# Kernel optimization log

Measured on AMD Instinct MI355X. Metric: run time of the kernel, lower is better.

## Reference

```python
import jax, jax.numpy as jnp
import numpy as np

TILE = 128
NEG = -1e10


def rotate_half(x):
    half = x.shape[-1] // 2
    return jnp.concatenate([-x[..., half:], x[..., :half]], axis=-1)


def setup_inputs() -> dict:
    key = jax.random.key(0)
    ks = jax.random.split(key, 7)
    B, S, E, H, D, K = 1, 4096, 2048, 16, 128, 8
    T = S // TILE
    x = jax.random.normal(ks[0], (B, S, E), jnp.float32)
    wq = jax.random.normal(ks[1], (E, H * D), jnp.float32) * 0.02
    wk = jax.random.normal(ks[2], (E, H * D), jnp.float32) * 0.02
    wv = jax.random.normal(ks[3], (E, H * D), jnp.float32) * 0.02
    wo = jax.random.normal(ks[4], (H * D, E), jnp.float32) * 0.02
    rope_angles = jax.random.uniform(ks[5], (S, D // 2), jnp.float32)
    anchor_indices = jax.random.randint(ks[6], (B, H, T, K), 0, T).astype(jnp.int32)
    return {"x": x, "wq": wq, "wk": wk, "wv": wv, "wo": wo,
            "rope_angles": rope_angles, "anchor_indices": anchor_indices}


def reference(x, wq, wk, wv, wo, rope_angles, anchor_indices):
    B, S, E = x.shape
    D = rope_angles.shape[1] * 2          # head_dim
    H = wq.shape[1] // D                  # num_heads
    T = S // TILE                         # num_tiles
    sm_scale = 1.0 / jnp.sqrt(jnp.float32(D))

    # QKV projections -> [B, H, S, D]
    def proj(w):
        return (x @ w).reshape(B, S, H, D).transpose(0, 2, 1, 3).astype(jnp.float32)
    q, k, v = proj(wq), proj(wk), proj(wv)

    # RoPE (half-split / rotate_half format)
    cos = jnp.cos(rope_angles)[None, None]   # [1,1,S,D/2]
    sin = jnp.sin(rope_angles)[None, None]
    cos_f = jnp.concatenate([cos, cos], axis=-1)
    sin_f = jnp.concatenate([sin, sin], axis=-1)
    q = q * cos_f + rotate_half(q) * sin_f
    k = k * cos_f + rotate_half(k) * sin_f

    # Tile selection: anchor tiles + local (diagonal) tile -> [B,H,T,K+1]
    local = jnp.broadcast_to(jnp.arange(T, dtype=jnp.int32)[None, None, :, None], (B, H, T, 1))
    tile_sel = jnp.concatenate([anchor_indices, local], axis=-1)
    L = tile_sel.shape[-1] * TILE            # sparse_len
    token_idx = tile_sel[..., None] * TILE + jnp.arange(TILE, dtype=jnp.int32)[None, None, None, None, :]
    flat_idx = jnp.clip(token_idx.reshape(B, H, T, L), 0, S - 1)  # [B,H,T,L]

    # Gather selected KV tiles: [B,H,T,L,D]
    def gather(kv):
        return jnp.take_along_axis(kv, flat_idx.reshape(B, H, T * L, 1), axis=2).reshape(B, H, T, L, D)
    k_sp, v_sp = gather(k), gather(v)

    # Block-sparse attention per query tile
    q_t = q.reshape(B, H, T, TILE, D)
    logits = jnp.einsum('bhtqd,bhtkd->bhtqk', q_t, k_sp) * sm_scale
    q_pos = jnp.arange(S).reshape(T, TILE)
    future = flat_idx[:, :, :, None, :] > q_pos[None, None, :, :, None]  # causal mask on gathered keys
    logits = jnp.where(future, NEG, logits)
    w = jax.nn.softmax(logits, axis=-1)
    all_masked = jnp.all(future, axis=-1, keepdims=True)
    w = jnp.where(all_masked, 0.0, w)
    w = jnp.where(jnp.isnan(w), 0.0, w)
    out = jnp.einsum('bhtqk,bhtkd->bhtqd', w, v_sp)

    out = out.reshape(B, H, S, D).transpose(0, 2, 1, 3).reshape(B, S, H * D)
    return out @ wo
```

## Files before the change

### kernel.cpp

```cpp
#include <hip/hip_runtime.h>
#include <stdint.h>

typedef unsigned short u16;
typedef unsigned int u32;

#define S_LEN 4096
#define EMB 2048
#define NH 16
#define HD 128
#define HDTOT 2048
#define T_TILES 32
#define KANCH 8
#define SM_SCALE 0.088388347648318447f

typedef __bf16 bf16x8 __attribute__((ext_vector_type(8)));
typedef float f32x4 __attribute__((ext_vector_type(4)));

typedef const __attribute__((address_space(1))) u32 ga_u32;
typedef __attribute__((address_space(3))) u32 lds_u32;

__device__ __forceinline__ u16 f2bf(float f) {
  u32 b = __builtin_bit_cast(u32, f);
  b = (b + 0x7FFFu + ((b >> 16) & 1u)) >> 16;
  return (u16)b;
}
__device__ __forceinline__ float bf2f(u16 u) {
  return __builtin_bit_cast(float, ((u32)u) << 16);
}
__device__ __forceinline__ f32x4 mfma16(bf16x8 a, bf16x8 b, f32x4 c) {
  return __builtin_amdgcn_mfma_f32_16x16x32_bf16(a, b, c, 0, 0, 0);
}

#define ASM_LGKM0 do { asm volatile("s_waitcnt lgkmcnt(0)" ::: "memory"); \
                       __builtin_amdgcn_sched_barrier(0); } while (0)
#define ASM_VMC(n) do { asm volatile("s_waitcnt vmcnt(" #n ")" ::: "memory"); \
                        __builtin_amdgcn_sched_barrier(0); } while (0)

__global__ __launch_bounds__(256) void k_convert_x(const float* __restrict__ x,
                                                   u16* __restrict__ xb) {
  int i = (blockIdx.x * 256 + threadIdx.x) * 4;
  float4 v = *(const float4*)(x + i);
  ushort4 o;
  o.x = f2bf(v.x); o.y = f2bf(v.y); o.z = f2bf(v.z); o.w = f2bf(v.w);
  *(ushort4*)(xb + i) = o;
}

__global__ __launch_bounds__(256) void k_transpose_w(
    const float* __restrict__ w0, const float* __restrict__ w1,
    const float* __restrict__ w2, const float* __restrict__ w3,
    u16* __restrict__ o0, u16* __restrict__ o1,
    u16* __restrict__ o2, u16* __restrict__ o3) {
  const float* w; u16* o;
  if (blockIdx.z == 0)      { w = w0; o = o0; }
  else if (blockIdx.z == 1) { w = w1; o = o1; }
  else if (blockIdx.z == 2) { w = w2; o = o2; }
  else                      { w = w3; o = o3; }
  __shared__ float tile[64][68];
  int n0 = blockIdx.x * 64, k0 = blockIdx.y * 64;
  int tid = threadIdx.x;
  int r = tid >> 4, cq = (tid & 15) << 2;
  for (int p = 0; p < 4; ++p) {
    float4 v = *(const float4*)(w + (size_t)(k0 + r + p * 16) * EMB + n0 + cq);
    tile[r + p * 16][cq + 0] = v.x;
    tile[r + p * 16][cq + 1] = v.y;
    tile[r + p * 16][cq + 2] = v.z;
    tile[r + p * 16][cq + 3] = v.w;
  }
  __syncthreads();
  for (int p = 0; p < 4; ++p) {
    int rn = r + p * 16;
    ushort4 u;
    u.x = f2bf(tile[cq + 0][rn]);
    u.y = f2bf(tile[cq + 1][rn]);
    u.z = f2bf(tile[cq + 2][rn]);
    u.w = f2bf(tile[cq + 3][rn]);
    *(ushort4*)(o + (size_t)(n0 + rn) * EMB + k0 + cq) = u;
  }
}

__global__ __launch_bounds__(256) void k_transpose_v(const u16* __restrict__ v,
                                                     u16* __restrict__ vt) {
  __shared__ u16 tile[64][72];
  int n0 = blockIdx.x * 64, s0 = blockIdx.y * 64;
  int tid = threadIdx.x;
  int r = tid >> 4, cq = (tid & 15) << 2;
  for (int p = 0; p < 4; ++p) {
    ushort4 u = *(const ushort4*)(v + (size_t)(s0 + r + p * 16) * HDTOT + n0 + cq);
    tile[r + p * 16][cq + 0] = u.x;
    tile[r + p * 16][cq + 1] = u.y;
    tile[r + p * 16][cq + 2] = u.z;
    tile[r + p * 16][cq + 3] = u.w;
  }
  __syncthreads();
  for (int p = 0; p < 4; ++p) {
    int rn = r + p * 16;
    ushort4 o;
    o.x = tile[cq + 0][rn];
    o.y = tile[cq + 1][rn];
    o.z = tile[cq + 2][rn];
    o.w = tile[cq + 3][rn];
    *(ushort4*)(vt + (size_t)(n0 + rn) * S_LEN + s0 + cq) = o;
  }
}

template <bool BF16OUT>
__device__ __forceinline__ void gemm_body(const u16* __restrict__ A,
                                          const u16* __restrict__ Bt,
                                          void* __restrict__ Cv,
                                          int N, int K, int m0, int n0,
                                          u16* As, u16* Bs) {
  const int tid = threadIdx.x;
  const int lane = tid & 63, wave = tid >> 6;
  const int quad = lane >> 4, l16 = lane & 15;
  const int wm = (wave >> 1) * 64, wn = (wave & 1) * 64;
  f32x4 acc[4][4] = {};

  const int flat0 = wave * 1024 + lane * 16;
  for (int kt = 0; kt < K; kt += 32) {
    for (int half = 0; half < 2; ++half) {
      int flat = flat0 + half * 4096;
      int row = flat >> 6, colb = flat & 63;
      const char* ga = (const char*)A + ((size_t)(m0 + row) * K + kt) * 2 + colb;
      const char* gb = (const char*)Bt + ((size_t)(n0 + row) * K + kt) * 2 + colb;
      int loff = wave * 1024 + half * 4096;
      __builtin_amdgcn_global_load_lds((ga_u32*)ga, (lds_u32*)((char*)As + loff), 16, 0, 0);
      __builtin_amdgcn_global_load_lds((ga_u32*)gb, (lds_u32*)((char*)Bs + loff), 16, 0, 0);
    }
    __syncthreads();
    bf16x8 af[4], bfr[4];
    for (int mt = 0; mt < 4; ++mt)
      af[mt] = *(const bf16x8*)(As + (wm + mt * 16 + l16) * 32 + quad * 8);
    for (int nt = 0; nt < 4; ++nt)
      bfr[nt] = *(const bf16x8*)(Bs + (wn + nt * 16 + l16) * 32 + quad * 8);
    for (int mt = 0; mt < 4; ++mt)
      for (int nt = 0; nt < 4; ++nt)
        acc[mt][nt] = mfma16(af[mt], bfr[nt], acc[mt][nt]);
    __syncthreads();
  }
  for (int mt = 0; mt < 4; ++mt) {
    int row = m0 + wm + mt * 16 + quad * 4;
    for (int nt = 0; nt < 4; ++nt) {
      int col = n0 + wn + nt * 16 + l16;
      for (int r = 0; r < 4; ++r) {
        if (BF16OUT)
          ((u16*)Cv)[(size_t)(row + r) * N + col] = f2bf(acc[mt][nt][r]);
        else
          ((float*)Cv)[(size_t)(row + r) * N + col] = acc[mt][nt][r];
      }
    }
  }
}

template <bool BF16OUT>
__global__ __launch_bounds__(256) void k_gemm(const u16* __restrict__ A,
                                              const u16* __restrict__ Bt,
                                              void* __restrict__ Cv,
                                              int N, int K) {
  __shared__ __align__(16) u16 As[128 * 32];
  __shared__ __align__(16) u16 Bs[128 * 32];
  gemm_body<BF16OUT>(A, Bt, Cv, N, K, blockIdx.y * 128, blockIdx.x * 128, As, Bs);
}

__global__ __launch_bounds__(512, 2) void k_gemm256_qkv(
    const u16* __restrict__ A, const u16* __restrict__ Bt,
    u16* __restrict__ q, u16* __restrict__ k, u16* __restrict__ v) {
  __shared__ __align__(16) u16 lds[65536];
  int flat = blockIdx.y * 24 + blockIdx.x;
  flat = (flat & 7) * 48 + (flat >> 3);
  const int bx = flat % 24, by = flat / 24;
  const int m0 = by * 256;
  const int n0g = bx * 256;
  u16* out = (bx < 8) ? q : ((bx < 16) ? k : v);
  const int ncol0 = (bx & 7) * 256;

  const int tid = threadIdx.x;
  const int lane = tid & 63, wave = tid >> 6;
  const int quad = lane >> 4, l16 = lane & 15;
  const int wm = wave >> 2, wn = wave & 3;
  const int sw0 = (quad ^ (l16 & 7)) * 8, sw1 = ((quad ^ (l16 & 7)) ^ 4) * 8;

  size_t soff[2];
#pragma unroll
  for (int p = 0; p < 2; ++p) {
    int fl = p * 8192 + tid * 16;
    int row = fl >> 7;
    int gsw = ((fl >> 4) & 7) ^ (row & 7);
    soff[p] = (size_t)row * 4096 + (size_t)(gsw * 16);
  }
  const char* aBase = (const char*)A + (size_t)m0 * 4096;
  const char* bBase = (const char*)Bt + (size_t)n0g * 4096;
  const int dstW = wave * 1024;

  auto stA = [&](int buf, int half, int kt) {
#pragma unroll
    for (int p = 0; p < 2; ++p)
      __builtin_amdgcn_global_load_lds(
          (ga_u32*)(aBase + (size_t)half * 524288 + (size_t)kt * 128 + soff[p]),
          (lds_u32*)((char*)lds + buf * 32768 + half * 16384 + p * 8192 + dstW),
          16, 0, 0);
  };
  auto stB = [&](int buf, int half, int kt) {
#pragma unroll
    for (int p = 0; p < 2; ++p)
      __builtin_amdgcn_global_load_lds(
          (ga_u32*)(bBase + (size_t)half * 524288 + (size_t)kt * 128 + soff[p]),
          (lds_u32*)((char*)lds + 65536 + buf * 32768 + half * 16384 + p * 8192 + dstW),
          16, 0, 0);
  };
  const u16* aRd = lds + wm * 8192 + l16 * 64;
  const u16* bRd = lds + 32768 + (wn >> 1) * 8192 + ((wn & 1) * 64 + l16) * 64;

  f32x4 acc[8][4] = {};

  stB(0, 0, 0); stA(0, 0, 0); stB(0, 1, 0); stA(0, 1, 0);
  stB(1, 0, 1); stA(1, 0, 1);
  ASM_VMC(4);
  __builtin_amdgcn_s_barrier();

  const int NT = EMB / 64;
  for (int j = 0; j < NT; ++j) {
    const int par = j & 1;
    const u16* aT = aRd + par * 16384;
    const u16* bT = bRd + par * 16384;
    bf16x8 af[4][2], blo[2][2], bhi[2][2];
#pragma unroll
    for (int m = 0; m < 4; ++m) {
      af[m][0] = *(const bf16x8*)(aT + m * 1024 + sw0);
      af[m][1] = *(const bf16x8*)(aT + m * 1024 + sw1);
    }
#pragma unroll
    for (int n = 0; n < 2; ++n) {
      blo[n][0] = *(const bf16x8*)(bT + n * 1024 + sw0);
      blo[n][1] = *(const bf16x8*)(bT + n * 1024 + sw1);
    }
    if (j + 1 < NT) stB(1 - par, 1, j + 1);
    __builtin_amdgcn_s_barrier();
    ASM_LGKM0;
    __builtin_amdgcn_s_setprio(1);
#pragma unroll
    for (int m = 0; m < 4; ++m)
#pragma unroll
      for (int n = 0; n < 2; ++n) {
        acc[m][n] = mfma16(af[m][0], blo[n][0], acc[m][n]);
        acc[m][n] = mfma16(af[m][1], blo[n][1], acc[m][n]);
      }
    __builtin_amdgcn_s_setprio(0);
    __builtin_amdgcn_s_barrier();
#pragma unroll
    for (int n = 0; n < 2; ++n) {
      bhi[n][0] = *(const bf16x8*)(bT + (n + 2) * 1024 + sw0);
      bhi[n][1] = *(const bf16x8*)(bT + (n + 2) * 1024 + sw1);
    }
    if (j + 1 < NT) stA(1 - par, 1, j + 1);
    __builtin_amdgcn_s_barrier();
    ASM_LGKM0;
    __builtin_amdgcn_s_setprio(1);
#pragma unroll
    for (int m = 0; m < 4; ++m)
#pragma unroll
      for (int n = 0; n < 2; ++n) {
        acc[m][n + 2] = mfma16(af[m][0], bhi[n][0], acc[m][n + 2]);
        acc[m][n + 2] = mfma16(af[m][1], bhi[n][1], acc[m][n + 2]);
      }
    __builtin_amdgcn_s_setprio(0);
    __builtin_amdgcn_s_barrier();
#pragma unroll
    for (int m = 0; m < 4; ++m) {
      af[m][0] = *(const bf16x8*)(aT + (m + 4) * 1024 + sw0);
      af[m][1] = *(const bf16x8*)(aT + (m + 4) * 1024 + sw1);
    }
    if (j + 2 < NT) stB(par, 0, j + 2);
    __builtin_amdgcn_s_barrier();
    ASM_LGKM0;
    __builtin_amdgcn_s_setprio(1);
#pragma unroll
    for (int m = 0; m < 4; ++m)
#pragma unroll
      for (int n = 0; n < 2; ++n) {
        acc[m + 4][n + 2] = mfma16(af[m][0], bhi[n][0], acc[m + 4][n + 2]);
        acc[m + 4][n + 2] = mfma16(af[m][1], bhi[n][1], acc[m + 4][n + 2]);
      }
    __builtin_amdgcn_s_setprio(0);
    __builtin_amdgcn_s_barrier();
    if (j + 2 < NT) stA(par, 0, j + 2);
    __builtin_amdgcn_s_barrier();
    __builtin_amdgcn_s_setprio(1);
#pragma unroll
    for (int m = 0; m < 4; ++m)
#pragma unroll
      for (int n = 0; n < 2; ++n) {
        acc[m + 4][n] = mfma16(af[m][0], blo[n][0], acc[m + 4][n]);
        acc[m + 4][n] = mfma16(af[m][1], blo[n][1], acc[m + 4][n]);
      }
    __builtin_amdgcn_s_setprio(0);
    if (j == NT - 2) { ASM_VMC(0); } else { ASM_VMC(4); }
    __builtin_amdgcn_s_barrier();
  }
#pragma unroll
  for (int m = 0; m < 8; ++m) {
    int row = m0 + wm * 128 + m * 16 + quad * 4;
#pragma unroll
    for (int n = 0; n < 4; ++n) {
      int col = ncol0 + wn * 64 + n * 16 + l16;
#pragma unroll
      for (int r = 0; r < 4; ++r)
        out[(size_t)(row + r) * HDTOT + col] = f2bf(acc[m][n][r]);
    }
  }
}

__global__ __launch_bounds__(256) void k_rope(u16* __restrict__ q, u16* __restrict__ k,
                                              const float* __restrict__ ang) {
  int gid = blockIdx.x * 256 + threadIdx.x;
  int s = gid >> 7;
  int h = (gid >> 3) & (NH - 1);
  int dq = (gid & 7) << 3;
  const float* ap = ang + s * 64 + dq;
  float4 a0 = *(const float4*)(ap);
  float4 a1 = *(const float4*)(ap + 4);
  float sn[8], cs[8];
  __sincosf(a0.x, &sn[0], &cs[0]);
  __sincosf(a0.y, &sn[1], &cs[1]);
  __sincosf(a0.z, &sn[2], &cs[2]);
  __sincosf(a0.w, &sn[3], &cs[3]);
  __sincosf(a1.x, &sn[4], &cs[4]);
  __sincosf(a1.y, &sn[5], &cs[5]);
  __sincosf(a1.z, &sn[6], &cs[6]);
  __sincosf(a1.w, &sn[7], &cs[7]);
  size_t base = (size_t)s * HDTOT + h * HD + dq;
  u16* ptrs[2] = {q, k};
#pragma unroll
  for (int a = 0; a < 2; ++a) {
    u16* p = ptrs[a] + base;
    ushort4 x1a = *(const ushort4*)(p);
    ushort4 x1b = *(const ushort4*)(p + 4);
    ushort4 x2a = *(const ushort4*)(p + 64);
    ushort4 x2b = *(const ushort4*)(p + 68);
    u16 v1[8] = {x1a.x, x1a.y, x1a.z, x1a.w, x1b.x, x1b.y, x1b.z, x1b.w};
    u16 v2[8] = {x2a.x, x2a.y, x2a.z, x2a.w, x2b.x, x2b.y, x2b.z, x2b.w};
    u16 o1[8], o2[8];
#pragma unroll
    for (int e = 0; e < 8; ++e) {
      float f1 = bf2f(v1[e]), f2 = bf2f(v2[e]);
      o1[e] = f2bf(f1 * cs[e] - f2 * sn[e]);
      o2[e] = f2bf(f2 * cs[e] + f1 * sn[e]);
    }
    *(ushort4*)(p)      = make_ushort4(o1[0], o1[1], o1[2], o1[3]);
    *(ushort4*)(p + 4)  = make_ushort4(o1[4], o1[5], o1[6], o1[7]);
    *(ushort4*)(p + 64) = make_ushort4(o2[0], o2[1], o2[2], o2[3]);
    *(ushort4*)(p + 68) = make_ushort4(o2[4], o2[5], o2[6], o2[7]);
  }
}

__device__ __forceinline__ bf16x8 ldsfrag(const u16* __restrict__ sbuf, int r, int cb) {
  return *(const bf16x8*)(sbuf + r * 128 + (((cb ^ (r & 15)) << 3)));
}
__device__ __forceinline__ bf16x8 ldsfragV(const u16* __restrict__ sbuf, int r, int cb) {
  return *(const bf16x8*)(sbuf + r * 64 + (((cb ^ (r & 7)) << 3)));
}

__global__ __launch_bounds__(512, 4) void k_attn(const u16* __restrict__ q,
                                                 const u16* __restrict__ k,
                                                 const u16* __restrict__ vt,
                                                 const int* __restrict__ anch,
                                                 u16* __restrict__ out) {
  __shared__ __align__(16) u16 bufK[2][64 * 128];
  __shared__ __align__(16) u16 bufV[2][128 * 64];
  __shared__ int s_tj[KANCH + 1];
  __shared__ int s_nv;
  const int xx = blockIdx.x, yy = blockIdx.y;
  const int h = (yy & 7) | ((xx & 1) << 3);
  const int t = (yy & 8) ? ((xx >> 1) << 1) : (T_TILES - 1 - ((xx >> 1) << 1));
  const int tid = threadIdx.x;
  const int lane = tid & 63, wave = tid >> 6;
  const int quad = lane >> 4, l16 = lane & 15;
  const int wq0 = wave * 16;

  int offK[2], offV[2];
#pragma unroll
  for (int p = 0; p < 2; ++p) {
    int krow = (wave * 2 + p) * 4 + (lane >> 4);
    int kcol = ((lane & 15) ^ (krow & 15)) << 3;
    offK[p] = (krow * HDTOT + kcol) * 2;
    int vrow = (wave * 2 + p) * 8 + (lane >> 3);
    int vcol = ((lane & 7) ^ (vrow & 7)) << 3;
    offV[p] = (vrow * S_LEN + vcol) * 2;
  }

  if (tid == 0) {
    int nv = 0;
    for (int j = 0; j < KANCH; ++j) {
      int tj = anch[((h * T_TILES) + t) * KANCH + j];
      if (tj <= t) s_tj[nv++] = tj;
    }
    s_tj[nv++] = t;
    s_nv = nv;
  }

  {
    const char* gq = (const char*)(q + (size_t)(t * 128) * HDTOT + h * HD);
    char* lq = (char*)bufK + wave * 4096;
#pragma unroll
    for (int p = 0; p < 4; ++p) {
      int qrow = (wave * 4 + p) * 4 + (lane >> 4);
      int qcol = ((lane & 15) ^ (qrow & 15)) << 3;
      __builtin_amdgcn_global_load_lds((ga_u32*)(gq + (qrow * HDTOT + qcol) * 2),
                                       (lds_u32*)(lq + p * 1024), 16, 0, 0);
    }
  }
  __syncthreads();

  bf16x8 qf[4];
#pragma unroll
  for (int ks = 0; ks < 4; ++ks)
    qf[ks] = ldsfrag(&bufK[0][0], wq0 + l16, ks * 4 + quad);

  const int nv2 = 2 * s_nv;
  const char* kh = (const char*)(k + h * HD);
  const char* vh = (const char*)(vt + (size_t)(h * HD) * S_LEN);

  __syncthreads();

  {
    int key0 = s_tj[0] * 128;
    const char* gk = kh + (size_t)key0 * (HDTOT * 2);
    const char* gv = vh + (size_t)key0 * 2;
    char* lk = (char*)bufK[0] + wave * 2048;
    char* lv = (char*)bufV[0] + wave * 2048;
#pragma unroll
    for (int p = 0; p < 2; ++p) {
      __builtin_amdgcn_global_load_lds((ga_u32*)(gk + offK[p]),
                                       (lds_u32*)(lk + p * 1024), 16, 0, 0);
      __builtin_amdgcn_global_load_lds((ga_u32*)(gv + offV[p]),
                                       (lds_u32*)(lv + p * 1024), 16, 0, 0);
    }
  }

  f32x4 oacc[8] = {};
  float m_st = -1e30f, l_st = 0.f;

  for (int i = 0; i < nv2; ++i) {
    const int par = i & 1;
    const u16* K_c = bufK[par];
    const u16* V_c = bufV[par];
    const int tj = s_tj[i >> 1];
    const int half = i & 1;
    const bool diag = (tj == t);

    __syncthreads();

    if (i + 1 < nv2) {
      int inx = i + 1;
      int key0 = s_tj[inx >> 1] * 128 + (inx & 1) * 64;
      const char* gk = kh + (size_t)key0 * (HDTOT * 2);
      const char* gv = vh + (size_t)key0 * 2;
      char* lk = (char*)bufK[1 - par] + wave * 2048;
      char* lv = (char*)bufV[1 - par] + wave * 2048;
#pragma unroll
      for (int p = 0; p < 2; ++p) {
        __builtin_amdgcn_global_load_lds((ga_u32*)(gk + offK[p]),
                                         (lds_u32*)(lk + p * 1024), 16, 0, 0);
        __builtin_amdgcn_global_load_lds((ga_u32*)(gv + offV[p]),
                                         (lds_u32*)(lv + p * 1024), 16, 0, 0);
      }
    }

    f32x4 sacc[4] = {};
#pragma unroll
    for (int ks = 0; ks < 4; ++ks)
#pragma unroll
      for (int a = 0; a < 4; ++a) {
        bf16x8 kf = ldsfrag(K_c, a * 16 + l16, ks * 4 + quad);
        sacc[a] = mfma16(kf, qf[ks], sacc[a]);
      }

    u32 pl[4], ph[4];
    float alpha;
    {
      const int qr = wq0 + l16;
      const int kb = half * 64;
      float rmax = -1e30f;
#pragma unroll
      for (int a = 0; a < 4; ++a) {
        f32x4 s4 = sacc[a];
#pragma unroll
        for (int r = 0; r < 4; ++r) {
          float sv = s4[r] * SM_SCALE;
          if (diag && (kb + a * 16 + quad * 4 + r > qr)) sv = -1e30f;
          s4[r] = sv;
          rmax = fmaxf(rmax, sv);
        }
        sacc[a] = s4;
      }
      rmax = fmaxf(rmax, __shfl_xor(rmax, 16));
      rmax = fmaxf(rmax, __shfl_xor(rmax, 32));
      float mnew = fmaxf(m_st, rmax);
      alpha = __expf(m_st - mnew);
      m_st = mnew;
      float rsum = 0.f;
#pragma unroll
      for (int a = 0; a < 4; ++a) {
        f32x4 s4 = sacc[a];
        float p0 = __expf(s4[0] - mnew);
        float p1 = __expf(s4[1] - mnew);
        float p2 = __expf(s4[2] - mnew);
        float p3 = __expf(s4[3] - mnew);
        rsum += (p0 + p1) + (p2 + p3);
        pl[a] = __builtin_amdgcn_perm(__builtin_bit_cast(u32, p1) + 0x8000u,
                                      __builtin_bit_cast(u32, p0) + 0x8000u,
                                      0x07060302u);
        ph[a] = __builtin_amdgcn_perm(__builtin_bit_cast(u32, p3) + 0x8000u,
                                      __builtin_bit_cast(u32, p2) + 0x8000u,
                                      0x07060302u);
      }
      rsum += __shfl_xor(rsum, 16);
      rsum += __shfl_xor(rsum, 32);
      l_st = l_st * alpha + rsum;
    }

    {
      f32x4 av;
#pragma unroll
      for (int r = 0; r < 4; ++r)
        av[r] = __shfl(alpha, (lane & 48) | (quad * 4 + r));
#pragma unroll
      for (int nt = 0; nt < 8; ++nt) {
        f32x4 o4 = oacc[nt];
        o4[0] *= av[0]; o4[1] *= av[1]; o4[2] *= av[2]; o4[3] *= av[3];
        oacc[nt] = o4;
      }
    }

    const int srcA = ((quad & 1) << 5) + l16;
    const int srcB = srcA + 16;
    const int hi = quad >> 1;
#pragma unroll
    for (int c = 0; c < 2; ++c) {
      u32 x0 = __shfl(pl[2 * c], srcA), x1 = __shfl(ph[2 * c], srcA);
      u32 x2 = __shfl(pl[2 * c], srcB), x3 = __shfl(ph[2 * c], srcB);
      u32 y0 = __shfl(pl[2 * c + 1], srcA), y1 = __shfl(ph[2 * c + 1], srcA);
      u32 y2 = __shfl(pl[2 * c + 1], srcB), y3 = __shfl(ph[2 * c + 1], srcB);
      uint4 w;
      w.x = hi ? y0 : x0;
      w.y = hi ? y1 : x1;
      w.z = hi ? y2 : x2;
      w.w = hi ? y3 : x3;
      bf16x8 pa = __builtin_bit_cast(bf16x8, w);
#pragma unroll
      for (int nt = 0; nt < 8; ++nt) {
        bf16x8 vf = ldsfragV(V_c, nt * 16 + l16, c * 4 + quad);
        oacc[nt] = mfma16(pa, vf, oacc[nt]);
      }
    }
  }

  {
    float linv = 1.0f / l_st;
    f32x4 iv;
#pragma unroll
    for (int r = 0; r < 4; ++r)
      iv[r] = __shfl(linv, (lane & 48) | (quad * 4 + r));
#pragma unroll
    for (int r = 0; r < 4; ++r) {
      size_t srow_o = (size_t)(t * 128 + wq0 + quad * 4 + r);
#pragma unroll
      for (int nt = 0; nt < 8; ++nt)
        out[srow_o * HDTOT + h * HD + nt * 16 + l16] = f2bf(oacc[nt][r] * iv[r]);
    }
  }
}

extern "C" void kernel_launch(void* const* d_in, const int* in_sizes, int n_in,
                              void* d_out, int out_size, void* d_ws, size_t ws_size,
                              hipStream_t stream) {
  const float* x   = (const float*)d_in[0];
  const float* wq  = (const float*)d_in[1];
  const float* wk  = (const float*)d_in[2];
  const float* wv  = (const float*)d_in[3];
  const float* wo  = (const float*)d_in[4];
  const float* ang = (const float*)d_in[5];
  const int* anch  = (const int*)d_in[6];

  char* ws = (char*)d_ws;
  const size_t SZ_SE = (size_t)S_LEN * HDTOT * sizeof(u16);
  const size_t SZ_W  = (size_t)EMB * EMB * sizeof(u16);
  u16* xb   = (u16*)(ws);
  u16* qb   = (u16*)(ws + SZ_SE);
  u16* kb   = (u16*)(ws + 2 * SZ_SE);
  u16* vb   = (u16*)(ws + 3 * SZ_SE);
  u16* vtb  = (u16*)(ws + 4 * SZ_SE);
  u16* attn = (u16*)(ws + 5 * SZ_SE);
  u16* wqT  = (u16*)(ws + 6 * SZ_SE);
  u16* wkT  = (u16*)(ws + 6 * SZ_SE + SZ_W);
  u16* wvT  = (u16*)(ws + 6 * SZ_SE + 2 * SZ_W);
  u16* woT  = (u16*)(ws + 6 * SZ_SE + 3 * SZ_W);

  k_convert_x<<<8192, 256, 0, stream>>>(x, xb);
  k_transpose_w<<<dim3(32, 32, 4), 256, 0, stream>>>(wq, wk, wv, wo, wqT, wkT, wvT, woT);
  k_gemm256_qkv<<<dim3(24, 16), 512, 0, stream>>>(xb, wqT, qb, kb, vb);
  k_rope<<<2048, 256, 0, stream>>>(qb, kb, ang);
  k_transpose_v<<<dim3(32, 64), 256, 0, stream>>>(vb, vtb);
  k_attn<<<dim3(T_TILES, NH), 512, 0, stream>>>(qb, kb, vtb, anch, attn);
  k_gemm<false><<<dim3(16, 32), 256, 0, stream>>>(attn, woT, d_out, EMB, HDTOT);
}
```

Measured before the change: 383.6 us.

## Fuse RoPE into QKV GEMM epilogue and restructure prefetch schedule

Removes the separate RoPE kernel. Q and K tiles are now staged through LDS as fp32 in the GEMM epilogue, and the rotation is applied there before the bf16 store, which avoids a round trip of Q and K through global memory and one launch. The prefetch schedule also changes: both halves of the next-next B and A tiles are issued together in later phases, and the vmcnt wait depth goes from 4 to 8. The risks are less even load interleaving within the loop and a longer epilogue with extra syncs and LDS traffic.

```diff
diff --git a/kernel.cpp b/kernel.cpp
--- a/kernel.cpp
+++ b/kernel.cpp
@@ -163,7 +163,8 @@
 
 __global__ __launch_bounds__(512, 2) void k_gemm256_qkv(
     const u16* __restrict__ A, const u16* __restrict__ Bt,
-    u16* __restrict__ q, u16* __restrict__ k, u16* __restrict__ v) {
+    u16* __restrict__ q, u16* __restrict__ k, u16* __restrict__ v,
+    const float* __restrict__ ang) {
   __shared__ __align__(16) u16 lds[65536];
   int flat = blockIdx.y * 24 + blockIdx.x;
   flat = (flat & 7) * 48 + (flat >> 3);
@@ -212,9 +213,9 @@
 
   f32x4 acc[8][4] = {};
 
-  stB(0, 0, 0); stA(0, 0, 0); stB(0, 1, 0); stA(0, 1, 0);
-  stB(1, 0, 1); stA(1, 0, 1);
-  ASM_VMC(4);
+  stB(0, 0, 0); stB(0, 1, 0); stA(0, 0, 0); stA(0, 1, 0);
+  stB(1, 0, 1); stB(1, 1, 1); stA(1, 0, 1); stA(1, 1, 1);
+  ASM_VMC(8);
   __builtin_amdgcn_s_barrier();
 
   const int NT = EMB / 64;
@@ -233,7 +234,6 @@
       blo[n][0] = *(const bf16x8*)(bT + n * 1024 + sw0);
       blo[n][1] = *(const bf16x8*)(bT + n * 1024 + sw1);
     }
-    if (j + 1 < NT) stB(1 - par, 1, j + 1);
     __builtin_amdgcn_s_barrier();
     ASM_LGKM0;
     __builtin_amdgcn_s_setprio(1);
@@ -251,7 +251,6 @@
       bhi[n][0] = *(const bf16x8*)(bT + (n + 2) * 1024 + sw0);
       bhi[n][1] = *(const bf16x8*)(bT + (n + 2) * 1024 + sw1);
     }
-    if (j + 1 < NT) stA(1 - par, 1, j + 1);
     __builtin_amdgcn_s_barrier();
     ASM_LGKM0;
     __builtin_amdgcn_s_setprio(1);
@@ -269,7 +268,7 @@
       af[m][0] = *(const bf16x8*)(aT + (m + 4) * 1024 + sw0);
       af[m][1] = *(const bf16x8*)(aT + (m + 4) * 1024 + sw1);
     }
-    if (j + 2 < NT) stB(par, 0, j + 2);
+    if (j + 2 < NT) { stB(par, 0, j + 2); stB(par, 1, j + 2); }
     __builtin_amdgcn_s_barrier();
     ASM_LGKM0;
     __builtin_amdgcn_s_setprio(1);
@@ -282,7 +281,7 @@
       }
     __builtin_amdgcn_s_setprio(0);
     __builtin_amdgcn_s_barrier();
-    if (j + 2 < NT) stA(par, 0, j + 2);
+    if (j + 2 < NT) { stA(par, 0, j + 2); stA(par, 1, j + 2); }
     __builtin_amdgcn_s_barrier();
     __builtin_amdgcn_s_setprio(1);
 #pragma unroll
@@ -293,62 +292,71 @@
         acc[m + 4][n] = mfma16(af[m][1], blo[n][1], acc[m + 4][n]);
       }
     __builtin_amdgcn_s_setprio(0);
-    if (j == NT - 2) { ASM_VMC(0); } else { ASM_VMC(4); }
-    __builtin_amdgcn_s_barrier();
-  }
-#pragma unroll
-  for (int m = 0; m < 8; ++m) {
-    int row = m0 + wm * 128 + m * 16 + quad * 4;
-#pragma unroll
-    for (int n = 0; n < 4; ++n) {
-      int col = ncol0 + wn * 64 + n * 16 + l16;
-#pragma unroll
-      for (int r = 0; r < 4; ++r)
-        out[(size_t)(row + r) * HDTOT + col] = f2bf(acc[m][n][r]);
-    }
-  }
-}
-
-__global__ __launch_bounds__(256) void k_rope(u16* __restrict__ q, u16* __restrict__ k,
-                                              const float* __restrict__ ang) {
-  int gid = blockIdx.x * 256 + threadIdx.x;
-  int s = gid >> 7;
-  int h = (gid >> 3) & (NH - 1);
-  int dq = (gid & 7) << 3;
-  const float* ap = ang + s * 64 + dq;
-  float4 a0 = *(const float4*)(ap);
-  float4 a1 = *(const float4*)(ap + 4);
-  float sn[8], cs[8];
-  __sincosf(a0.x, &sn[0], &cs[0]);
-  __sincosf(a0.y, &sn[1], &cs[1]);
-  __sincosf(a0.z, &sn[2], &cs[2]);
-  __sincosf(a0.w, &sn[3], &cs[3]);
-  __sincosf(a1.x, &sn[4], &cs[4]);
-  __sincosf(a1.y, &sn[5], &cs[5]);
-  __sincosf(a1.z, &sn[6], &cs[6]);
-  __sincosf(a1.w, &sn[7], &cs[7]);
-  size_t base = (size_t)s * HDTOT + h * HD + dq;
-  u16* ptrs[2] = {q, k};
-#pragma unroll
-  for (int a = 0; a < 2; ++a) {
-    u16* p = ptrs[a] + base;
-    ushort4 x1a = *(const ushort4*)(p);
-    ushort4 x1b = *(const ushort4*)(p + 4);
-    ushort4 x2a = *(const ushort4*)(p + 64);
-    ushort4 x2b = *(const ushort4*)(p + 68);
-    u16 v1[8] = {x1a.x, x1a.y, x1a.z, x1a.w, x1b.x, x1b.y, x1b.z, x1b.w};
-    u16 v2[8] = {x2a.x, x2a.y, x2a.z, x2a.w, x2b.x, x2b.y, x2b.z, x2b.w};
-    u16 o1[8], o2[8];
-#pragma unroll
-    for (int e = 0; e < 8; ++e) {
-      float f1 = bf2f(v1[e]), f2 = bf2f(v2[e]);
-      o1[e] = f2bf(f1 * cs[e] - f2 * sn[e]);
-      o2[e] = f2bf(f2 * cs[e] + f1 * sn[e]);
-    }
-    *(ushort4*)(p)      = make_ushort4(o1[0], o1[1], o1[2], o1[3]);
-    *(ushort4*)(p + 4)  = make_ushort4(o1[4], o1[5], o1[6], o1[7]);
-    *(ushort4*)(p + 64) = make_ushort4(o2[0], o2[1], o2[2], o2[3]);
-    *(ushort4*)(p + 68) = make_ushort4(o2[4], o2[5], o2[6], o2[7]);
+    if (j == NT - 2) { ASM_VMC(0); } else { ASM_VMC(8); }
+    __builtin_amdgcn_s_barrier();
+  }
+
+  if (bx < 16) {
+    float* lf = (float*)lds;
+#pragma unroll
+    for (int mh = 0; mh < 2; ++mh) {
+      __syncthreads();
+#pragma unroll
+      for (int mm = 0; mm < 4; ++mm) {
+        int lrow0 = wm * 64 + mm * 16 + quad * 4;
+#pragma unroll
+        for (int n = 0; n < 4; ++n) {
+          int col = wn * 64 + n * 16 + l16;
+#pragma unroll
+          for (int r = 0; r < 4; ++r)
+            lf[(lrow0 + r) * 256 + (col ^ (quad << 4))] = acc[mh * 4 + mm][n][r];
+        }
+      }
+      __syncthreads();
+#pragma unroll
+      for (int ii = 0; ii < 8; ++ii) {
+        int idx = ii * 512 + tid;
+        int lrow = idx >> 5;
+        int lq = idx & 31;
+        int head = lq >> 4;
+        int dq = (lq & 15) << 2;
+        int clo = head * 128 + dq;
+        int sgn = (lrow >> 2) & 3;
+        float4 x1 = *(const float4*)&lf[lrow * 256 + (clo ^ (sgn << 4))];
+        float4 x2 = *(const float4*)&lf[lrow * 256 + ((clo + 64) ^ (sgn << 4))];
+        int row_g = m0 + ((lrow >> 6) * 128) + mh * 64 + (lrow & 63);
+        float4 a = *(const float4*)(ang + (size_t)row_g * 64 + dq);
+        float sn0, cs0, sn1, cs1, sn2, cs2, sn3, cs3;
+        __sincosf(a.x, &sn0, &cs0);
+        __sincosf(a.y, &sn1, &cs1);
+        __sincosf(a.z, &sn2, &cs2);
+        __sincosf(a.w, &sn3, &cs3);
+        ushort4 olo, ohi;
+        olo.x = f2bf(x1.x * cs0 - x2.x * sn0);
+        olo.y = f2bf(x1.y * cs1 - x2.y * sn1);
+        olo.z = f2bf(x1.z * cs2 - x2.z * sn2);
+        olo.w = f2bf(x1.w * cs3 - x2.w * sn3);
+        ohi.x = f2bf(x2.x * cs0 + x1.x * sn0);
+        ohi.y = f2bf(x2.y * cs1 + x1.y * sn1);
+        ohi.z = f2bf(x2.z * cs2 + x1.z * sn2);
+        ohi.w = f2bf(x2.w * cs3 + x1.w * sn3);
+        u16* op = out + (size_t)row_g * HDTOT + ncol0 + clo;
+        *(ushort4*)op = olo;
+        *(ushort4*)(op + 64) = ohi;
+      }
+    }
+  } else {
+#pragma unroll
+    for (int m = 0; m < 8; ++m) {
+      int row = m0 + wm * 128 + m * 16 + quad * 4;
+#pragma unroll
+      for (int n = 0; n < 4; ++n) {
+        int col = ncol0 + wn * 64 + n * 16 + l16;
+#pragma unroll
+        for (int r = 0; r < 4; ++r)
+          out[(size_t)(row + r) * HDTOT + col] = f2bf(acc[m][n][r]);
+      }
+    }
   }
 }
 
@@ -597,8 +605,7 @@
 
   k_convert_x<<<8192, 256, 0, stream>>>(x, xb);
   k_transpose_w<<<dim3(32, 32, 4), 256, 0, stream>>>(wq, wk, wv, wo, wqT, wkT, wvT, woT);
-  k_gemm256_qkv<<<dim3(24, 16), 512, 0, stream>>>(xb, wqT, qb, kb, vb);
-  k_rope<<<2048, 256, 0, stream>>>(qb, kb, ang);
+  k_gemm256_qkv<<<dim3(24, 16), 512, 0, stream>>>(xb, wqT, qb, kb, vb, ang);
   k_transpose_v<<<dim3(32, 64), 256, 0, stream>>>(vb, vtb);
   k_attn<<<dim3(T_TILES, NH), 512, 0, stream>>>(qb, kb, vtb, anch, attn);
   k_gemm<false><<<dim3(16, 32), 256, 0, stream>>>(attn, woT, d_out, EMB, HDTOT);
```

Result: no change. 386.6 us (+0.8%).

## Fuse RoPE into QKV GEMM epilogue with precomputed sincos table

Applied to the files above, without the earlier changes.

Removes the standalone RoPE kernel by remapping the B-fragment column layout so each wave holds paired d and d+64 columns, applying the rotation in the QKV GEMM epilogue from a precomputed cos/sin table. The table is built by a small new kernel and stored temporarily in the output buffer, which is overwritten later by the final GEMM. The attention launch grid is also remapped to a 1D ordering that pairs heavy and light causal tiles. This saves a read-modify-write pass over Q and K, at the cost of scattered per-element table loads in the epilogue.

```diff
diff --git a/kernel.cpp b/kernel.cpp
--- a/kernel.cpp
+++ b/kernel.cpp
@@ -35,6 +35,15 @@
                        __builtin_amdgcn_sched_barrier(0); } while (0)
 #define ASM_VMC(n) do { asm volatile("s_waitcnt vmcnt(" #n ")" ::: "memory"); \
                         __builtin_amdgcn_sched_barrier(0); } while (0)
+
+__global__ __launch_bounds__(256) void k_sincos(const float* __restrict__ ang,
+                                                float2* __restrict__ tab) {
+  int i = blockIdx.x * 256 + threadIdx.x;
+  float a = ang[i];
+  float s, c;
+  __sincosf(a, &s, &c);
+  tab[i] = make_float2(c, s);
+}
 
 __global__ __launch_bounds__(256) void k_convert_x(const float* __restrict__ x,
                                                    u16* __restrict__ xb) {
@@ -163,7 +172,8 @@
 
 __global__ __launch_bounds__(512, 2) void k_gemm256_qkv(
     const u16* __restrict__ A, const u16* __restrict__ Bt,
-    u16* __restrict__ q, u16* __restrict__ k, u16* __restrict__ v) {
+    u16* __restrict__ q, u16* __restrict__ k, u16* __restrict__ v,
+    const float2* __restrict__ cssn) {
   __shared__ __align__(16) u16 lds[65536];
   int flat = blockIdx.y * 24 + blockIdx.x;
   flat = (flat & 7) * 48 + (flat >> 3);
@@ -208,7 +218,7 @@
           16, 0, 0);
   };
   const u16* aRd = lds + wm * 8192 + l16 * 64;
-  const u16* bRd = lds + 32768 + (wn >> 1) * 8192 + ((wn & 1) * 64 + l16) * 64;
+  const u16* bRd = lds + 32768 + (wn * 16 + l16) * 64;
 
   f32x4 acc[8][4] = {};
 
@@ -230,8 +240,8 @@
     }
 #pragma unroll
     for (int n = 0; n < 2; ++n) {
-      blo[n][0] = *(const bf16x8*)(bT + n * 1024 + sw0);
-      blo[n][1] = *(const bf16x8*)(bT + n * 1024 + sw1);
+      blo[n][0] = *(const bf16x8*)(bT + n * 4096 + sw0);
+      blo[n][1] = *(const bf16x8*)(bT + n * 4096 + sw1);
     }
     if (j + 1 < NT) stB(1 - par, 1, j + 1);
     __builtin_amdgcn_s_barrier();
@@ -248,8 +258,8 @@
     __builtin_amdgcn_s_barrier();
 #pragma unroll
     for (int n = 0; n < 2; ++n) {
-      bhi[n][0] = *(const bf16x8*)(bT + (n + 2) * 1024 + sw0);
-      bhi[n][1] = *(const bf16x8*)(bT + (n + 2) * 1024 + sw1);
+      bhi[n][0] = *(const bf16x8*)(bT + (n + 2) * 4096 + sw0);
+      bhi[n][1] = *(const bf16x8*)(bT + (n + 2) * 4096 + sw1);
     }
     if (j + 1 < NT) stA(1 - par, 1, j + 1);
     __builtin_amdgcn_s_barrier();
@@ -296,59 +306,37 @@
     if (j == NT - 2) { ASM_VMC(0); } else { ASM_VMC(4); }
     __builtin_amdgcn_s_barrier();
   }
-#pragma unroll
-  for (int m = 0; m < 8; ++m) {
-    int row = m0 + wm * 128 + m * 16 + quad * 4;
-#pragma unroll
-    for (int n = 0; n < 4; ++n) {
-      int col = ncol0 + wn * 64 + n * 16 + l16;
-#pragma unroll
-      for (int r = 0; r < 4; ++r)
-        out[(size_t)(row + r) * HDTOT + col] = f2bf(acc[m][n][r]);
-    }
-  }
-}
-
-__global__ __launch_bounds__(256) void k_rope(u16* __restrict__ q, u16* __restrict__ k,
-                                              const float* __restrict__ ang) {
-  int gid = blockIdx.x * 256 + threadIdx.x;
-  int s = gid >> 7;
-  int h = (gid >> 3) & (NH - 1);
-  int dq = (gid & 7) << 3;
-  const float* ap = ang + s * 64 + dq;
-  float4 a0 = *(const float4*)(ap);
-  float4 a1 = *(const float4*)(ap + 4);
-  float sn[8], cs[8];
-  __sincosf(a0.x, &sn[0], &cs[0]);
-  __sincosf(a0.y, &sn[1], &cs[1]);
-  __sincosf(a0.z, &sn[2], &cs[2]);
-  __sincosf(a0.w, &sn[3], &cs[3]);
-  __sincosf(a1.x, &sn[4], &cs[4]);
-  __sincosf(a1.y, &sn[5], &cs[5]);
-  __sincosf(a1.z, &sn[6], &cs[6]);
-  __sincosf(a1.w, &sn[7], &cs[7]);
-  size_t base = (size_t)s * HDTOT + h * HD + dq;
-  u16* ptrs[2] = {q, k};
-#pragma unroll
-  for (int a = 0; a < 2; ++a) {
-    u16* p = ptrs[a] + base;
-    ushort4 x1a = *(const ushort4*)(p);
-    ushort4 x1b = *(const ushort4*)(p + 4);
-    ushort4 x2a = *(const ushort4*)(p + 64);
-    ushort4 x2b = *(const ushort4*)(p + 68);
-    u16 v1[8] = {x1a.x, x1a.y, x1a.z, x1a.w, x1b.x, x1b.y, x1b.z, x1b.w};
-    u16 v2[8] = {x2a.x, x2a.y, x2a.z, x2a.w, x2b.x, x2b.y, x2b.z, x2b.w};
-    u16 o1[8], o2[8];
-#pragma unroll
-    for (int e = 0; e < 8; ++e) {
-      float f1 = bf2f(v1[e]), f2 = bf2f(v2[e]);
-      o1[e] = f2bf(f1 * cs[e] - f2 * sn[e]);
-      o2[e] = f2bf(f2 * cs[e] + f1 * sn[e]);
-    }
-    *(ushort4*)(p)      = make_ushort4(o1[0], o1[1], o1[2], o1[3]);
-    *(ushort4*)(p + 4)  = make_ushort4(o1[4], o1[5], o1[6], o1[7]);
-    *(ushort4*)(p + 64) = make_ushort4(o2[0], o2[1], o2[2], o2[3]);
-    *(ushort4*)(p + 68) = make_ushort4(o2[4], o2[5], o2[6], o2[7]);
+
+  if (bx < 16) {
+    const int dcol = wn * 16 + l16;
+#pragma unroll
+    for (int m = 0; m < 8; ++m) {
+      int srow = m0 + wm * 128 + m * 16 + quad * 4;
+#pragma unroll
+      for (int r = 0; r < 4; ++r) {
+        int s = srow + r;
+        float2 cs2 = cssn[s * 64 + dcol];
+        u16* op = out + (size_t)s * HDTOT + ncol0 + dcol;
+        float lo0 = acc[m][0][r], hi0 = acc[m][1][r];
+        op[0]   = f2bf(lo0 * cs2.x - hi0 * cs2.y);
+        op[64]  = f2bf(hi0 * cs2.x + lo0 * cs2.y);
+        float lo1 = acc[m][2][r], hi1 = acc[m][3][r];
+        op[128] = f2bf(lo1 * cs2.x - hi1 * cs2.y);
+        op[192] = f2bf(hi1 * cs2.x + lo1 * cs2.y);
+      }
+    }
+  } else {
+#pragma unroll
+    for (int m = 0; m < 8; ++m) {
+      int row = m0 + wm * 128 + m * 16 + quad * 4;
+#pragma unroll
+      for (int n = 0; n < 4; ++n) {
+        int col = ncol0 + (wn + 4 * n) * 16 + l16;
+#pragma unroll
+        for (int r = 0; r < 4; ++r)
+          out[(size_t)(row + r) * HDTOT + col] = f2bf(acc[m][n][r]);
+      }
+    }
   }
 }
 
@@ -368,9 +356,11 @@
   __shared__ __align__(16) u16 bufV[2][128 * 64];
   __shared__ int s_tj[KANCH + 1];
   __shared__ int s_nv;
-  const int xx = blockIdx.x, yy = blockIdx.y;
-  const int h = (yy & 7) | ((xx & 1) << 3);
-  const int t = (yy & 8) ? ((xx >> 1) << 1) : (T_TILES - 1 - ((xx >> 1) << 1));
+  const int i = blockIdx.x;
+  const int p2 = (i ^ (i >> 8)) & 1;
+  const int c = i >> 1;
+  const int t = p2 ? (15 - (c >> 4)) : (16 + (c >> 4));
+  const int h = c & 15;
   const int tid = threadIdx.x;
   const int lane = tid & 63, wave = tid >> 6;
   const int quad = lane >> 4, l16 = lane & 15;
@@ -439,18 +429,18 @@
   f32x4 oacc[8] = {};
   float m_st = -1e30f, l_st = 0.f;
 
-  for (int i = 0; i < nv2; ++i) {
-    const int par = i & 1;
+  for (int it = 0; it < nv2; ++it) {
+    const int par = it & 1;
     const u16* K_c = bufK[par];
     const u16* V_c = bufV[par];
-    const int tj = s_tj[i >> 1];
-    const int half = i & 1;
+    const int tj = s_tj[it >> 1];
+    const int half = it & 1;
     const bool diag = (tj == t);
 
     __syncthreads();
 
-    if (i + 1 < nv2) {
-      int inx = i + 1;
+    if (it + 1 < nv2) {
+      int inx = it + 1;
       int key0 = s_tj[inx >> 1] * 128 + (inx & 1) * 64;
       const char* gk = kh + (size_t)key0 * (HDTOT * 2);
       const char* gv = vh + (size_t)key0 * 2;
@@ -535,11 +525,11 @@
     const int srcB = srcA + 16;
     const int hi = quad >> 1;
 #pragma unroll
-    for (int c = 0; c < 2; ++c) {
-      u32 x0 = __shfl(pl[2 * c], srcA), x1 = __shfl(ph[2 * c], srcA);
-      u32 x2 = __shfl(pl[2 * c], srcB), x3 = __shfl(ph[2 * c], srcB);
-      u32 y0 = __shfl(pl[2 * c + 1], srcA), y1 = __shfl(ph[2 * c + 1], srcA);
-      u32 y2 = __shfl(pl[2 * c + 1], srcB), y3 = __shfl(ph[2 * c + 1], srcB);
+    for (int cc = 0; cc < 2; ++cc) {
+      u32 x0 = __shfl(pl[2 * cc], srcA), x1 = __shfl(ph[2 * cc], srcA);
+      u32 x2 = __shfl(pl[2 * cc], srcB), x3 = __shfl(ph[2 * cc], srcB);
+      u32 y0 = __shfl(pl[2 * cc + 1], srcA), y1 = __shfl(ph[2 * cc + 1], srcA);
+      u32 y2 = __shfl(pl[2 * cc + 1], srcB), y3 = __shfl(ph[2 * cc + 1], srcB);
       uint4 w;
       w.x = hi ? y0 : x0;
       w.y = hi ? y1 : x1;
@@ -548,7 +538,7 @@
       bf16x8 pa = __builtin_bit_cast(bf16x8, w);
 #pragma unroll
       for (int nt = 0; nt < 8; ++nt) {
-        bf16x8 vf = ldsfragV(V_c, nt * 16 + l16, c * 4 + quad);
+        bf16x8 vf = ldsfragV(V_c, nt * 16 + l16, cc * 4 + quad);
         oacc[nt] = mfma16(pa, vf, oacc[nt]);
       }
     }
@@ -595,11 +585,13 @@
   u16* wvT  = (u16*)(ws + 6 * SZ_SE + 2 * SZ_W);
   u16* woT  = (u16*)(ws + 6 * SZ_SE + 3 * SZ_W);
 
+  float2* cssn = (float2*)d_out;
+
+  k_sincos<<<1024, 256, 0, stream>>>(ang, cssn);
   k_convert_x<<<8192, 256, 0, stream>>>(x, xb);
   k_transpose_w<<<dim3(32, 32, 4), 256, 0, stream>>>(wq, wk, wv, wo, wqT, wkT, wvT, woT);
-  k_gemm256_qkv<<<dim3(24, 16), 512, 0, stream>>>(xb, wqT, qb, kb, vb);
-  k_rope<<<2048, 256, 0, stream>>>(qb, kb, ang);
+  k_gemm256_qkv<<<dim3(24, 16), 512, 0, stream>>>(xb, wqT, qb, kb, vb, cssn);
   k_transpose_v<<<dim3(32, 64), 256, 0, stream>>>(vb, vtb);
-  k_attn<<<dim3(T_TILES, NH), 512, 0, stream>>>(qb, kb, vtb, anch, attn);
+  k_attn<<<dim3(512), 512, 0, stream>>>(qb, kb, vtb, anch, attn);
   k_gemm<false><<<dim3(16, 32), 256, 0, stream>>>(attn, woT, d_out, EMB, HDTOT);
 }
```

New measurement: 382.2 us. Within noise of the previous version (-0.4%).
